# Performance work log

Measured on AMD Instinct MI355X. Metric: run time of the kernel, lower is better.

## Reference

```python
import jax, jax.numpy as jnp
import numpy as np

T, B, V, H = 2048, 32, 512, 512


def setup_inputs() -> dict:
    key = jax.random.key(0)
    ks = jax.random.split(key, 7)
    s = 1.0 / np.sqrt(V + H)  # torch nn.Linear default init bound
    u = lambda k, shape: jax.random.uniform(k, shape, jnp.float32, -s, s)
    return {
        "inputs": jax.random.normal(ks[0], (T, B, V), jnp.float32),
        "state": jnp.zeros((1, B, H), jnp.float32),
        "W_reset": u(ks[1], (V + H, H)),
        "b_reset": u(ks[2], (H,)),
        "W_net": u(ks[3], (V + H, H)),
        "b_net": u(ks[4], (H,)),
        "W_update": u(ks[5], (V + H, H)),
        "b_update": u(ks[6], (H,)),
    }


def reference(inputs, state, W_reset, b_reset, W_net, b_net, W_update, b_update):
    # inputs: [T, B, V], state: [1, B, H]
    h0 = state[0]  # [B, H]

    def step(h, x):
        # x: [B, V], h: [B, H]
        xh = jnp.concatenate([x, h], axis=-1)               # [B, V+H]
        R = jax.nn.sigmoid(xh @ W_reset + b_reset)          # [B, H]
        xr = jnp.concatenate([x, h * R], axis=-1)           # [B, V+H]
        H_t = jnp.tanh(xr @ W_net + b_net)                  # candidate
        Z = jax.nn.sigmoid(xr @ W_update + b_update)        # NOTE: from (x, h*R), faithful to source
        h_new = Z * h + (1.0 - Z) * H_t
        return h_new, h_new

    h_final, states = jax.lax.scan(step, h0, inputs)        # states: [T, B, H]
    return states, h_final[None]                            # ([T,B,H], [1,B,H])
```

## Files before the change

### kernel.cpp

```cpp
#include <hip/hip_runtime.h>
#include <cstdint>
#include <cstddef>

#define T_STEPS 2048
#define BATCH   32
#define VDIM    512
#define HDIM    512
#define SLICES  8
#define COLS    64
#define KPT     64
#define BM      128
#define BN      64

typedef _Float16 half2v __attribute__((ext_vector_type(2)));
typedef _Float16 half8v __attribute__((ext_vector_type(8)));
typedef float    f32x4  __attribute__((ext_vector_type(4)));

__device__ __forceinline__ float dot2h(half2v a, half2v b, float c) {
#if __has_builtin(__builtin_amdgcn_fdot2)
    return __builtin_amdgcn_fdot2(a, b, c, false);
#else
    return fmaf((float)a.x, (float)b.x, fmaf((float)a.y, (float)b.y, c));
#endif
}

__device__ __forceinline__ unsigned long long loadt(const unsigned long long* p) {
    return __hip_atomic_load(p, __ATOMIC_RELAXED, __HIP_MEMORY_SCOPE_AGENT);
}
__device__ __forceinline__ void storet(unsigned long long* p, float v, unsigned tag) {
    unsigned long long x = ((unsigned long long)tag << 32) | (unsigned)__float_as_uint(v);
    __hip_atomic_store(p, x, __ATOMIC_RELAXED, __HIP_MEMORY_SCOPE_AGENT);
}

__global__ __launch_bounds__(512)
void pack_b(const float* __restrict__ W0, const float* __restrict__ W1,
            const float* __restrict__ W2, _Float16* __restrict__ Bt)
{
    const int kg = blockIdx.x;
    const int g  = blockIdx.y;
    const float* W = (g == 0) ? W0 : (g == 1) ? W1 : W2;
    const int n = threadIdx.x;
    half8v v;
    #pragma unroll
    for (int i = 0; i < 8; ++i)
        v[i] = (_Float16)W[(size_t)(kg * 8 + i) * HDIM + n];
    *(half8v*)&Bt[((((size_t)g * 64 + kg) * 512) + n) * 8] = v;
}

__global__ __launch_bounds__(256)
void xproj_mfma2(const float* __restrict__ X, const _Float16* __restrict__ Bt,
                 const float* __restrict__ b0, const float* __restrict__ b1,
                 const float* __restrict__ b2,
                 float* __restrict__ xp, int M)
{
    const int n0 = blockIdx.x * BN;
    const int m0 = blockIdx.y * BM;

    __shared__ __align__(16) _Float16 Blds[64 * 64 * 8];

    const int tid  = threadIdx.x;
    const int lane = tid & 63;
    const int w    = tid >> 6;
    const int r16  = lane & 15;
    const int kq   = lane >> 4;

    half8v a[2][16];
    #pragma unroll
    for (int ms = 0; ms < 2; ++ms) {
        const float* ap = X + (size_t)(m0 + 32 * w + 16 * ms + r16) * VDIM;
        #pragma unroll
        for (int ks = 0; ks < 16; ++ks) {
            const float* p = ap + ks * 32 + kq * 8;
            float4 x0 = *(const float4*)p;
            float4 x1 = *(const float4*)(p + 4);
            half8v v;
            v[0] = (_Float16)x0.x; v[1] = (_Float16)x0.y;
            v[2] = (_Float16)x0.z; v[3] = (_Float16)x0.w;
            v[4] = (_Float16)x1.x; v[5] = (_Float16)x1.y;
            v[6] = (_Float16)x1.z; v[7] = (_Float16)x1.w;
            a[ms][ks] = v;
        }
    }
    #pragma unroll
    for (int ms = 0; ms < 2; ++ms)
        #pragma unroll
        for (int ks = 0; ks < 16; ++ks)
            asm volatile("" : "+v"(a[ms][ks]));

    for (int g = 0; g < 3; ++g) {
        __syncthreads();
        {
            const _Float16* src = Bt + (((size_t)g * 64) * 512 + n0) * 8;
            const int c = tid & 63;
            #pragma unroll
            for (int it = 0; it < 16; ++it) {
                const int kg = (tid >> 6) + 4 * it;
                *(half8v*)&Blds[(size_t)(kg * 64 + c) * 8] =
                    *(const half8v*)&src[((size_t)kg * 512 + c) * 8];
            }
        }
        __syncthreads();

        f32x4 acc[2][4] = {};
        #pragma unroll
        for (int ks = 0; ks < 16; ++ks) {
            #pragma unroll
            for (int cb = 0; cb < 4; ++cb) {
                half8v bf = *(const half8v*)
                    &Blds[(size_t)((4 * ks + kq) * 64 + 16 * cb + r16) * 8];
                acc[0][cb] = __builtin_amdgcn_mfma_f32_16x16x32_f16(a[0][ks], bf, acc[0][cb], 0, 0, 0);
                acc[1][cb] = __builtin_amdgcn_mfma_f32_16x16x32_f16(a[1][ks], bf, acc[1][cb], 0, 0, 0);
            }
        }

        const float* bias = (g == 0) ? b0 : (g == 1) ? b1 : b2;
        float* out = xp + (size_t)g * M * HDIM;
        #pragma unroll
        for (int cb = 0; cb < 4; ++cb) {
            const float bb = bias[n0 + 16 * cb + r16];
            #pragma unroll
            for (int ms = 0; ms < 2; ++ms)
                #pragma unroll
                for (int r = 0; r < 4; ++r) {
                    const int row = m0 + 32 * w + 16 * ms + 4 * kq + r;
                    out[(size_t)row * HDIM + n0 + 16 * cb + r16] = acc[ms][cb][r] + bb;
                }
        }
    }
}

__global__ __launch_bounds__(512)
__attribute__((amdgpu_waves_per_eu(2, 2)))
void gru_scan6(const float* __restrict__ xp,
               const float* __restrict__ Wrh, const float* __restrict__ Wnh,
               const float* __restrict__ Wzh,
               const float* __restrict__ state, float* __restrict__ out,
               unsigned long long* __restrict__ hT,
               unsigned long long* __restrict__ uT,
               int t0, int nt, int M)
{
    const int b   = blockIdx.x & (BATCH - 1);
    const int s   = blockIdx.x >> 5;
    const int tid = threadIdx.x;
    const int c   = tid & (COLS - 1);
    const int j   = tid >> 6;
    const int n   = s * COLS + c;

    __shared__ __align__(16) _Float16 hlds[HDIM];
    __shared__ __align__(16) _Float16 ulds[HDIM];
    __shared__ float redR[SLICES][COLS];
    __shared__ float redN[SLICES][COLS];
    __shared__ float redZ[SLICES][COLS];

    half2v w2r[KPT / 2], w2n[KPT / 2], w2z[KPT / 2];
    {
        const size_t coloff = (size_t)s * COLS + c;
        const float* pr = Wrh + (size_t)j * KPT * HDIM + coloff;
        const float* pn = Wnh + (size_t)j * KPT * HDIM + coloff;
        const float* pz = Wzh + (size_t)j * KPT * HDIM + coloff;
        #pragma unroll
        for (int q = 0; q < KPT / 2; ++q) {
            half2v r, nn, z;
            r.x  = (_Float16)pr[(size_t)(2 * q) * HDIM];
            r.y  = (_Float16)pr[(size_t)(2 * q + 1) * HDIM];
            nn.x = (_Float16)pn[(size_t)(2 * q) * HDIM];
            nn.y = (_Float16)pn[(size_t)(2 * q + 1) * HDIM];
            z.x  = (_Float16)pz[(size_t)(2 * q) * HDIM];
            z.y  = (_Float16)pz[(size_t)(2 * q + 1) * HDIM];
            w2r[q] = r; w2n[q] = nn; w2z[q] = z;
        }
        #pragma unroll
        for (int q = 0; q < KPT / 2; ++q)
            asm volatile("" : "+v"(w2r[q]), "+v"(w2n[q]), "+v"(w2z[q]));
    }

    const size_t bb32 = (size_t)b * HDIM;
    unsigned long long* hTb = hT + bb32;
    unsigned long long* uTb = uT + bb32;
    const size_t gs = (size_t)M * HDIM;

    float hcv = 0.f;

    for (int tt = 0; tt < nt; ++tt) {
        const int t = t0 + tt;

        float xr = 0.f, xnn = 0.f, xz = 0.f;
        const size_t rb = ((size_t)tt * BATCH + b) * HDIM;
        if (tid < COLS) {
            xr  = xp[rb + n];
            xnn = xp[gs + rb + n];
            xz  = xp[2 * gs + rb + n];
        }

        float hv;
        if (t == 0) {
            hv = state[bb32 + tid];
            if (tid < COLS) hcv = state[bb32 + n];
        } else {
            unsigned long long v;
            do { v = loadt(hTb + tid); } while ((unsigned)(v >> 32) != (unsigned)t);
            hv = __uint_as_float((unsigned)v);
            if (tt == 0 && tid < COLS) {
                do { v = loadt(hTb + n); } while ((unsigned)(v >> 32) != (unsigned)t);
                hcv = __uint_as_float((unsigned)v);
            }
        }

        hlds[tid] = (_Float16)hv;
        asm volatile("s_waitcnt lgkmcnt(0)" ::: "memory");
        __builtin_amdgcn_sched_barrier(0);

        {
            float a0 = 0.f, a1 = 0.f, a2 = 0.f, a3 = 0.f;
            const half8v* hp = (const half8v*)&hlds[j * KPT];
            #pragma unroll
            for (int q = 0; q < KPT / 8; ++q) {
                half8v h8 = hp[q];
                half2v p0 = {h8[0], h8[1]}, p1 = {h8[2], h8[3]};
                half2v p2 = {h8[4], h8[5]}, p3 = {h8[6], h8[7]};
                a0 = dot2h(p0, w2r[4 * q + 0], a0);
                a1 = dot2h(p1, w2r[4 * q + 1], a1);
                a2 = dot2h(p2, w2r[4 * q + 2], a2);
                a3 = dot2h(p3, w2r[4 * q + 3], a3);
            }
            redR[j][c] = (a0 + a1) + (a2 + a3);
        }
        __syncthreads();

        if (tid < COLS) {
            float s01 = redR[0][c] + redR[1][c];
            float s23 = redR[2][c] + redR[3][c];
            float s45 = redR[4][c] + redR[5][c];
            float s67 = redR[6][c] + redR[7][c];
            float sR  = (s01 + s23) + (s45 + s67);
            float R = 1.f / (1.f + __expf(-(xr + sR)));
            storet(uTb + n, hcv * R, (unsigned)(t + 1));
        }

        {
            unsigned long long v;
            do { v = loadt(uTb + tid); } while ((unsigned)(v >> 32) != (unsigned)(t + 1));
            ulds[tid] = (_Float16)__uint_as_float((unsigned)v);
        }
        asm volatile("s_waitcnt lgkmcnt(0)" ::: "memory");
        __builtin_amdgcn_sched_barrier(0);

        {
            float aN0 = 0.f, aN1 = 0.f, aZ0 = 0.f, aZ1 = 0.f;
            const half8v* up = (const half8v*)&ulds[j * KPT];
            #pragma unroll
            for (int q = 0; q < KPT / 8; ++q) {
                half8v u8 = up[q];
                half2v p0 = {u8[0], u8[1]}, p1 = {u8[2], u8[3]};
                half2v p2 = {u8[4], u8[5]}, p3 = {u8[6], u8[7]};
                aN0 = dot2h(p0, w2n[4 * q + 0], aN0);
                aZ0 = dot2h(p0, w2z[4 * q + 0], aZ0);
                aN1 = dot2h(p1, w2n[4 * q + 1], aN1);
                aZ1 = dot2h(p1, w2z[4 * q + 1], aZ1);
                aN0 = dot2h(p2, w2n[4 * q + 2], aN0);
                aZ0 = dot2h(p2, w2z[4 * q + 2], aZ0);
                aN1 = dot2h(p3, w2n[4 * q + 3], aN1);
                aZ1 = dot2h(p3, w2z[4 * q + 3], aZ1);
            }
            redN[j][c] = aN0 + aN1;
            redZ[j][c] = aZ0 + aZ1;
        }
        __syncthreads();

        if (tid < COLS) {
            float n01 = redN[0][c] + redN[1][c], n23 = redN[2][c] + redN[3][c];
            float n45 = redN[4][c] + redN[5][c], n67 = redN[6][c] + redN[7][c];
            float z01 = redZ[0][c] + redZ[1][c], z23 = redZ[2][c] + redZ[3][c];
            float z45 = redZ[4][c] + redZ[5][c], z67 = redZ[6][c] + redZ[7][c];
            float sN = (n01 + n23) + (n45 + n67);
            float sZ = (z01 + z23) + (z45 + z67);
            float e  = __expf(2.f * (xnn + sN));
            float Hc = 1.f - 2.f / (e + 1.f);
            float Z  = 1.f / (1.f + __expf(-(xz + sZ)));
            float hnew = Z * hcv + (1.f - Z) * Hc;
            storet(hTb + n, hnew, (unsigned)(t + 1));
            __builtin_nontemporal_store(hnew, out + (size_t)t * BATCH * HDIM + bb32 + n);
            hcv = hnew;
            if (t == T_STEPS - 1)
                out[(size_t)T_STEPS * BATCH * HDIM + bb32 + n] = hnew;
        }
    }
}

extern "C" void kernel_launch(void* const* d_in, const int* in_sizes, int n_in,
                              void* d_out, int out_size, void* d_ws, size_t ws_size,
                              hipStream_t stream) {
    const float* inputs   = (const float*)d_in[0];
    const float* state    = (const float*)d_in[1];
    const float* W_reset  = (const float*)d_in[2];
    const float* b_reset  = (const float*)d_in[3];
    const float* W_net    = (const float*)d_in[4];
    const float* b_net    = (const float*)d_in[5];
    const float* W_update = (const float*)d_in[6];
    const float* b_update = (const float*)d_in[7];
    float* out = (float*)d_out;

    const size_t tag_bytes = 2ull * BATCH * HDIM * 8;
    const size_t bt_bytes  = 3ull * 64 * 512 * 8 * sizeof(_Float16);
    size_t tag_base = (ws_size - tag_bytes) & ~(size_t)255;
    size_t bt_base  = (tag_base - bt_bytes) & ~(size_t)255;
    char* base = (char*)d_ws;
    float*      xp = (float*)base;
    _Float16*   Bt = (_Float16*)(base + bt_base);
    unsigned long long* hT = (unsigned long long*)(base + tag_base);
    unsigned long long* uT = hT + (size_t)BATCH * HDIM;

    const size_t per_t = 3ull * BATCH * HDIM * sizeof(float);
    int C = (int)(bt_base / per_t);
    if (C > T_STEPS) C = T_STEPS;
    C &= ~3;
    if (C < 4) C = 4;

    hipMemsetAsync(hT, 0xFF, tag_bytes, stream);

    dim3 gp(64, 3);
    pack_b<<<gp, 512, 0, stream>>>(W_reset, W_net, W_update, Bt);

    for (int t0 = 0; t0 < T_STEPS; t0 += C) {
        const int nt = (T_STEPS - t0 < C) ? (T_STEPS - t0) : C;
        const int M  = nt * BATCH;

        dim3 g1(HDIM / BN, M / BM);
        xproj_mfma2<<<g1, 256, 0, stream>>>(inputs + (size_t)t0 * BATCH * VDIM,
                                            Bt, b_reset, b_net, b_update, xp, M);

        gru_scan6<<<BATCH * SLICES, 512, 0, stream>>>(
            xp,
            W_reset  + (size_t)VDIM * HDIM,
            W_net    + (size_t)VDIM * HDIM,
            W_update + (size_t)VDIM * HDIM,
            state, out, hT, uT, t0, nt, M);
    }
}
```

Measured before the change: 5.338 ms.

## Process four batch rows per scan block to reuse register-resident weights

The recurrent scan kernel now has each block handle four batch rows (KCH=4) instead of one, so the grid shrinks from 256 to 64 blocks. Each block holds the same fp16 weight slice in registers and reuses it across four batch vectors per timestep, with the LDS buffers and reduction arrays widened accordingly. This cuts the number of blocks that must each load the full weight slice and spreads the cross-block handshake over more work per block. The trade-off is four times more dot-product work per thread per step on fewer CUs, which lengthens the serial critical path of each timestep and increases polling traffic per block.

```diff
diff --git a/kernel.cpp b/kernel.cpp
--- a/kernel.cpp
+++ b/kernel.cpp
@@ -9,6 +9,7 @@
 #define SLICES  8
 #define COLS    64
 #define KPT     64
+#define KCH     4
 #define BM      128
 #define BN      64
 
@@ -131,7 +132,7 @@
 
 __global__ __launch_bounds__(512)
 __attribute__((amdgpu_waves_per_eu(2, 2)))
-void gru_scan6(const float* __restrict__ xp,
+void gru_scan7(const float* __restrict__ xp,
                const float* __restrict__ Wrh, const float* __restrict__ Wnh,
                const float* __restrict__ Wzh,
                const float* __restrict__ state, float* __restrict__ out,
@@ -139,25 +140,25 @@
                unsigned long long* __restrict__ uT,
                int t0, int nt, int M)
 {
-    const int b   = blockIdx.x & (BATCH - 1);
-    const int s   = blockIdx.x >> 5;
+    const int g   = blockIdx.x & 7;
+    const int s   = blockIdx.x >> 3;
     const int tid = threadIdx.x;
     const int c   = tid & (COLS - 1);
-    const int j   = tid >> 6;
+    const int jw  = tid >> 6;
     const int n   = s * COLS + c;
 
-    __shared__ __align__(16) _Float16 hlds[HDIM];
-    __shared__ __align__(16) _Float16 ulds[HDIM];
-    __shared__ float redR[SLICES][COLS];
-    __shared__ float redN[SLICES][COLS];
-    __shared__ float redZ[SLICES][COLS];
+    __shared__ __align__(16) _Float16 hlds[KCH][HDIM];
+    __shared__ __align__(16) _Float16 ulds[KCH][HDIM];
+    __shared__ float redR[KCH][SLICES][COLS];
+    __shared__ float redN[KCH][SLICES][COLS];
+    __shared__ float redZ[KCH][SLICES][COLS];
 
     half2v w2r[KPT / 2], w2n[KPT / 2], w2z[KPT / 2];
     {
         const size_t coloff = (size_t)s * COLS + c;
-        const float* pr = Wrh + (size_t)j * KPT * HDIM + coloff;
-        const float* pn = Wnh + (size_t)j * KPT * HDIM + coloff;
-        const float* pz = Wzh + (size_t)j * KPT * HDIM + coloff;
+        const float* pr = Wrh + (size_t)jw * KPT * HDIM + coloff;
+        const float* pn = Wnh + (size_t)jw * KPT * HDIM + coloff;
+        const float* pz = Wzh + (size_t)jw * KPT * HDIM + coloff;
         #pragma unroll
         for (int q = 0; q < KPT / 2; ++q) {
             half2v r, nn, z;
@@ -174,45 +175,59 @@
             asm volatile("" : "+v"(w2r[q]), "+v"(w2n[q]), "+v"(w2z[q]));
     }
 
-    const size_t bb32 = (size_t)b * HDIM;
-    unsigned long long* hTb = hT + bb32;
-    unsigned long long* uTb = uT + bb32;
     const size_t gs = (size_t)M * HDIM;
+    unsigned long long* hTb[KCH];
+    unsigned long long* uTb[KCH];
+    #pragma unroll
+    for (int i = 0; i < KCH; ++i) {
+        hTb[i] = hT + (size_t)(KCH * g + i) * HDIM;
+        uTb[i] = uT + (size_t)(KCH * g + i) * HDIM;
+    }
 
     float hcv = 0.f;
+    if (jw < KCH) {
+        if (t0 == 0) {
+            hcv = state[(size_t)(KCH * g + jw) * HDIM + n];
+        } else {
+            unsigned long long v;
+            do { v = loadt(hTb[jw] + n); } while ((unsigned)(v >> 32) != (unsigned)t0);
+            hcv = __uint_as_float((unsigned)v);
+        }
+    }
 
     for (int tt = 0; tt < nt; ++tt) {
         const int t = t0 + tt;
 
         float xr = 0.f, xnn = 0.f, xz = 0.f;
-        const size_t rb = ((size_t)tt * BATCH + b) * HDIM;
-        if (tid < COLS) {
-            xr  = xp[rb + n];
-            xnn = xp[gs + rb + n];
-            xz  = xp[2 * gs + rb + n];
-        }
-
-        float hv;
+        if (jw < KCH) {
+            const size_t rbj = ((size_t)tt * BATCH + (KCH * g + jw)) * HDIM;
+            xr  = xp[rbj + n];
+            xnn = xp[gs + rbj + n];
+            xz  = xp[2 * gs + rbj + n];
+        }
+
         if (t == 0) {
-            hv = state[bb32 + tid];
-            if (tid < COLS) hcv = state[bb32 + n];
+            #pragma unroll
+            for (int i = 0; i < KCH; ++i)
+                hlds[i][tid] = (_Float16)state[(size_t)(KCH * g + i) * HDIM + tid];
         } else {
-            unsigned long long v;
-            do { v = loadt(hTb + tid); } while ((unsigned)(v >> 32) != (unsigned)t);
-            hv = __uint_as_float((unsigned)v);
-            if (tt == 0 && tid < COLS) {
-                do { v = loadt(hTb + n); } while ((unsigned)(v >> 32) != (unsigned)t);
-                hcv = __uint_as_float((unsigned)v);
-            }
-        }
-
-        hlds[tid] = (_Float16)hv;
+            unsigned long long v[KCH];
+            #pragma unroll
+            for (int i = 0; i < KCH; ++i) v[i] = loadt(hTb[i] + tid);
+            #pragma unroll
+            for (int i = 0; i < KCH; ++i)
+                while ((unsigned)(v[i] >> 32) != (unsigned)t) v[i] = loadt(hTb[i] + tid);
+            #pragma unroll
+            for (int i = 0; i < KCH; ++i)
+                hlds[i][tid] = (_Float16)__uint_as_float((unsigned)v[i]);
+        }
         asm volatile("s_waitcnt lgkmcnt(0)" ::: "memory");
         __builtin_amdgcn_sched_barrier(0);
 
-        {
+        #pragma unroll
+        for (int i = 0; i < KCH; ++i) {
             float a0 = 0.f, a1 = 0.f, a2 = 0.f, a3 = 0.f;
-            const half8v* hp = (const half8v*)&hlds[j * KPT];
+            const half8v* hp = (const half8v*)&hlds[i][jw * KPT];
             #pragma unroll
             for (int q = 0; q < KPT / 8; ++q) {
                 half8v h8 = hp[q];
@@ -223,31 +238,38 @@
                 a2 = dot2h(p2, w2r[4 * q + 2], a2);
                 a3 = dot2h(p3, w2r[4 * q + 3], a3);
             }
-            redR[j][c] = (a0 + a1) + (a2 + a3);
+            redR[i][jw][c] = (a0 + a1) + (a2 + a3);
         }
         __syncthreads();
 
-        if (tid < COLS) {
-            float s01 = redR[0][c] + redR[1][c];
-            float s23 = redR[2][c] + redR[3][c];
-            float s45 = redR[4][c] + redR[5][c];
-            float s67 = redR[6][c] + redR[7][c];
+        if (jw < KCH) {
+            float s01 = redR[jw][0][c] + redR[jw][1][c];
+            float s23 = redR[jw][2][c] + redR[jw][3][c];
+            float s45 = redR[jw][4][c] + redR[jw][5][c];
+            float s67 = redR[jw][6][c] + redR[jw][7][c];
             float sR  = (s01 + s23) + (s45 + s67);
             float R = 1.f / (1.f + __expf(-(xr + sR)));
-            storet(uTb + n, hcv * R, (unsigned)(t + 1));
+            storet(uTb[jw] + n, hcv * R, (unsigned)(t + 1));
         }
 
         {
-            unsigned long long v;
-            do { v = loadt(uTb + tid); } while ((unsigned)(v >> 32) != (unsigned)(t + 1));
-            ulds[tid] = (_Float16)__uint_as_float((unsigned)v);
+            unsigned long long v[KCH];
+            #pragma unroll
+            for (int i = 0; i < KCH; ++i) v[i] = loadt(uTb[i] + tid);
+            #pragma unroll
+            for (int i = 0; i < KCH; ++i)
+                while ((unsigned)(v[i] >> 32) != (unsigned)(t + 1)) v[i] = loadt(uTb[i] + tid);
+            #pragma unroll
+            for (int i = 0; i < KCH; ++i)
+                ulds[i][tid] = (_Float16)__uint_as_float((unsigned)v[i]);
         }
         asm volatile("s_waitcnt lgkmcnt(0)" ::: "memory");
         __builtin_amdgcn_sched_barrier(0);
 
-        {
+        #pragma unroll
+        for (int i = 0; i < KCH; ++i) {
             float aN0 = 0.f, aN1 = 0.f, aZ0 = 0.f, aZ1 = 0.f;
-            const half8v* up = (const half8v*)&ulds[j * KPT];
+            const half8v* up = (const half8v*)&ulds[i][jw * KPT];
             #pragma unroll
             for (int q = 0; q < KPT / 8; ++q) {
                 half8v u8 = up[q];
@@ -262,27 +284,28 @@
                 aN1 = dot2h(p3, w2n[4 * q + 3], aN1);
                 aZ1 = dot2h(p3, w2z[4 * q + 3], aZ1);
             }
-            redN[j][c] = aN0 + aN1;
-            redZ[j][c] = aZ0 + aZ1;
+            redN[i][jw][c] = aN0 + aN1;
+            redZ[i][jw][c] = aZ0 + aZ1;
         }
         __syncthreads();
 
-        if (tid < COLS) {
-            float n01 = redN[0][c] + redN[1][c], n23 = redN[2][c] + redN[3][c];
-            float n45 = redN[4][c] + redN[5][c], n67 = redN[6][c] + redN[7][c];
-            float z01 = redZ[0][c] + redZ[1][c], z23 = redZ[2][c] + redZ[3][c];
-            float z45 = redZ[4][c] + redZ[5][c], z67 = redZ[6][c] + redZ[7][c];
+        if (jw < KCH) {
+            float n01 = redN[jw][0][c] + redN[jw][1][c], n23 = redN[jw][2][c] + redN[jw][3][c];
+            float n45 = redN[jw][4][c] + redN[jw][5][c], n67 = redN[jw][6][c] + redN[jw][7][c];
+            float z01 = redZ[jw][0][c] + redZ[jw][1][c], z23 = redZ[jw][2][c] + redZ[jw][3][c];
+            float z45 = redZ[jw][4][c] + redZ[jw][5][c], z67 = redZ[jw][6][c] + redZ[jw][7][c];
             float sN = (n01 + n23) + (n45 + n67);
             float sZ = (z01 + z23) + (z45 + z67);
             float e  = __expf(2.f * (xnn + sN));
             float Hc = 1.f - 2.f / (e + 1.f);
             float Z  = 1.f / (1.f + __expf(-(xz + sZ)));
             float hnew = Z * hcv + (1.f - Z) * Hc;
-            storet(hTb + n, hnew, (unsigned)(t + 1));
-            __builtin_nontemporal_store(hnew, out + (size_t)t * BATCH * HDIM + bb32 + n);
+            storet(hTb[jw] + n, hnew, (unsigned)(t + 1));
+            const size_t orow = ((size_t)t * BATCH + (KCH * g + jw)) * HDIM + n;
+            __builtin_nontemporal_store(hnew, out + orow);
             hcv = hnew;
             if (t == T_STEPS - 1)
-                out[(size_t)T_STEPS * BATCH * HDIM + bb32 + n] = hnew;
+                out[(size_t)T_STEPS * BATCH * HDIM + (size_t)(KCH * g + jw) * HDIM + n] = hnew;
         }
     }
 }
@@ -329,7 +352,7 @@
         xproj_mfma2<<<g1, 256, 0, stream>>>(inputs + (size_t)t0 * BATCH * VDIM,
                                             Bt, b_reset, b_net, b_update, xp, M);
 
-        gru_scan6<<<BATCH * SLICES, 512, 0, stream>>>(
+        gru_scan7<<<(BATCH / KCH) * SLICES, 512, 0, stream>>>(
             xp,
             W_reset  + (size_t)VDIM * HDIM,
             W_net    + (size_t)VDIM * HDIM,
```

Result: slower. 11.31 ms (+111.9%).
